# Kernel tuning notes

Measured on AMD Instinct MI355X. Metric: run time of the kernel, lower is better.

Reference implementation:

```python
import jax, jax.numpy as jnp
import numpy as np

NUM_NODES = 2048
NUM_UNITS = 64
INPUT_DIM = 2
MAX_K = 2  # max_diffusion_step


def setup_inputs() -> dict:
    key = jax.random.key(0)
    ks = jax.random.split(key, 8)
    B, N, U, D = 32, NUM_NODES, NUM_UNITS, INPUT_DIM
    C = D + U                      # input_size after concat = 66
    M = 2 * MAX_K + 1              # num_matrices = 5
    w_scale = 1.0 / np.sqrt(C * M)
    return {
        "inputs": jax.random.normal(ks[0], (B, N * D), dtype=jnp.float32),
        "hx": jax.random.normal(ks[1], (B, N * U), dtype=jnp.float32),
        # row-stochastic-ish random-walk supports (scaled so K hops stay bounded)
        "support0": jax.random.uniform(ks[2], (N, N), dtype=jnp.float32) / N,
        "support1": jax.random.uniform(ks[3], (N, N), dtype=jnp.float32) / N,
        "W_ru": jax.random.normal(ks[4], (C * M, 2 * U), dtype=jnp.float32) * w_scale,
        "b_ru": jnp.full((2 * U,), 1.0, dtype=jnp.float32),   # bias_start=1.0
        "W_c": jax.random.normal(ks[5], (C * M, U), dtype=jnp.float32) * w_scale,
        "b_c": jnp.zeros((U,), dtype=jnp.float32),            # bias_start=0.0
    }


def _gconv(inputs, state, supports, W, b, output_size):
    # inputs: [B, N*D], state: [B, N*U]
    B = inputs.shape[0]
    N = NUM_NODES
    x0 = jnp.concatenate(
        [inputs.reshape(B, N, -1), state.reshape(B, N, -1)], axis=2
    )  # [B, N, C]
    C = x0.shape[2]
    xs = [x0]
    for S in supports:  # Chebyshev-style diffusion per support
        x1 = jnp.einsum("nm,bmc->bnc", S, x0)
        xs.append(x1)
        xk1, xk2 = x1, x0
        for _ in range(2, MAX_K + 1):
            x2 = 2.0 * jnp.einsum("nm,bmc->bnc", S, xk1) - xk2
            xs.append(x2)
            xk1, xk2 = x2, xk1
    M = len(xs)  # num_matrices
    # stack on new leading axis then permute(1,2,3,0): feature-major, matrix-minor
    x = jnp.stack(xs, axis=0).transpose(1, 2, 3, 0).reshape(B * N, C * M)
    out = x @ W + b  # [B*N, output_size]
    return out.reshape(B, N * output_size)


def reference(inputs, hx, support0, support1, W_ru, b_ru, W_c, b_c):
    B = inputs.shape[0]
    N, U = NUM_NODES, NUM_UNITS
    supports = (support0, support1)
    value = jax.nn.sigmoid(_gconv(inputs, hx, supports, W_ru, b_ru, 2 * U))
    value = value.reshape(B, N, 2 * U)
    r = value[..., :U].reshape(B, N * U)
    u = value[..., U:].reshape(B, N * U)
    c = jnp.tanh(_gconv(inputs, r * hx, supports, W_c, b_c, U))
    new_state = u * hx + (1.0 - u) * c
    return new_state
```

## Files before the change

kernel.cpp:

```cpp
#include <hip/hip_runtime.h>
#include <hip/hip_bf16.h>
#include <cstdint>
#include <cstddef>

typedef unsigned short u16;
typedef unsigned char u8;
using f32x4 = __attribute__((ext_vector_type(4))) float;
using s16x8 = __attribute__((ext_vector_type(8))) short;
using s64x2 = __attribute__((ext_vector_type(2))) long;

#define NN 2048
#define BB 32
#define CC 66
#define JREAL 2112
#define JR 2176
#define KF 352
#define SROWS 65536

__device__ __forceinline__ int kperm(int k6) {
  return 16 * ((k6 >> 3) & 3) + 8 * (k6 >> 5) + (k6 & 7);
}

__device__ __forceinline__ float bf2f(u16 u) {
  union { uint32_t i; float f; } v; v.i = ((uint32_t)u) << 16; return v.f;
}
__device__ __forceinline__ u16 f2bf(float f) {
  union { float f; uint32_t i; } v; v.f = f;
  uint32_t x = v.i;
  x += 0x7fffu + ((x >> 16) & 1u);
  return (u16)(x >> 16);
}
__device__ __forceinline__ u8 f2e4m3(float x) {
  union { float f; uint32_t i; } v; v.f = x;
  uint32_t s = (v.i >> 24) & 0x80u;
  float a = fabsf(x);
  if (a >= 464.0f) return (u8)(s | 0x7Eu);
  if (a < 0.015625f) {
    int q = (int)rintf(a * 512.0f);
    return (u8)(s | (uint32_t)q);
  }
  union { float f; uint32_t i; } u; u.f = a;
  uint32_t lsb = (u.i >> 20) & 1u;
  u.i += 0x0007FFFFu + lsb;
  int e = (int)(u.i >> 23) - 127;
  uint32_t m = (u.i >> 20) & 7u;
  return (u8)(s | ((uint32_t)(e + 7) << 3) | m);
}

__device__ __forceinline__ void async_cp16(const u8* g, u8* l) {
  __builtin_amdgcn_global_load_lds(
      (const __attribute__((address_space(1))) unsigned int*)g,
      (__attribute__((address_space(3))) unsigned int*)l, 16, 0, 0);
}
__device__ __forceinline__ void async_cp16u(const u16* g, u16* l) {
  __builtin_amdgcn_global_load_lds(
      (const __attribute__((address_space(1))) unsigned int*)g,
      (__attribute__((address_space(3))) unsigned int*)l, 16, 0, 0);
}

template <int EPI>
__global__ __launch_bounds__(512, 2) void gemm_f8(
    const u8* __restrict__ A0, const u8* __restrict__ A1,
    const u8* __restrict__ A2, const u8* __restrict__ A3,
    const u8* __restrict__ B0, const u8* __restrict__ B1,
    const u8* __restrict__ B2, const u8* __restrict__ B3,
    void* __restrict__ C0, void* __restrict__ C1,
    void* __restrict__ C2, void* __restrict__ C3,
    int K, int lda, int ldb, int ldout, int mlimit)
{
  __shared__ u8 lds[3 * 25600];

  const int gx = gridDim.x, gy = gridDim.y;
  const int nwg = gx * gy * gridDim.z;
  const int orig = blockIdx.x + gx * (blockIdx.y + gy * blockIdx.z);
  const int cpx = nwg >> 3;
  const int swz = (orig & 7) * cpx + (orig >> 3);
  const int mb = swz % gx;
  const int t1 = swz / gx;
  const int nb = t1 % gy;
  const int zb = t1 / gy;

  const u8* A = (zb == 0) ? A0 : (zb == 1) ? A1 : (zb == 2) ? A2 : A3;
  const u8* B = (zb == 0) ? B0 : (zb == 1) ? B1 : (zb == 2) ? B2 : B3;
  void* Cv    = (zb == 0) ? C0 : (zb == 1) ? C1 : (zb == 2) ? C2 : C3;

  const int tid = threadIdx.x;
  const int wid = tid >> 6;
  const int lane = tid & 63;
  const int m0 = mb * 128;
  const int n0 = nb * 256;
  const int wm = (wid >> 2) * 64;
  const int wn = (wid & 3) * 64;

  const bool xtra = (EPI == 5) && (mb < 4);
  const int xrow0 = 2048 + mb * 16;
  const bool xw = xtra && (wid == 0);
  const bool xm = xtra && (wid < 4);

  const int srow = wid * 16 + (lane >> 2);
  const int sk   = ((lane & 3) ^ ((lane >> 3) & 3)) * 16;
  const u8* gA = A + (size_t)(m0 + srow) * lda + sk;
  const u8* gB = B + (size_t)(n0 + srow) * ldb + sk;
  const u8* gAx = A + (size_t)(xrow0 + (lane >> 2)) * lda + sk;
  u8* ldsA  = &lds[wid * 1024];
  u8* ldsB0 = &lds[8192 + wid * 1024];
  u8* ldsB1 = &lds[16384 + wid * 1024];
  u8* ldsAx = &lds[24576];

  const int r16 = lane & 15;
  const int hi = lane >> 4;
  const int rq = (r16 >> 1) & 3;
  const int goff = (hi ^ rq) * 16;
  const int abase = (wm + r16) * 64 + goff;
  const int bbase = 8192 + (wn + r16) * 64 + goff;
  const int xbase = 24576 + r16 * 64 + goff;

  f32x4 acc[4][4] = {};
  f32x4 accx[4] = {};
  const int nt = K >> 6;

#define STAGE_ALL(T_, SO_) { const int k0_ = (T_) * 64;                      \
    async_cp16(gA + k0_, ldsA + (SO_));                                      \
    async_cp16(gB + k0_, ldsB0 + (SO_));                                     \
    async_cp16(gB + (size_t)128 * ldb + k0_, ldsB1 + (SO_));                 \
    if (xw) async_cp16(gAx + k0_, ldsAx + (SO_)); }

  STAGE_ALL(0, 0);
  STAGE_ALL(1, 25600);
  if (xw) { asm volatile("s_waitcnt vmcnt(4)" ::: "memory"); }
  else    { asm volatile("s_waitcnt vmcnt(3)" ::: "memory"); }
  __builtin_amdgcn_s_barrier();

  int scur = 0;
  for (int t = 0; t < nt; ++t) {
    const int soff = scur * 25600;
    const bool more = (t + 2) < nt;
    int sst = scur + 2; if (sst >= 3) sst -= 3;
    const int so2 = sst * 25600;
    const int k2 = (t + 2) * 64;

    s64x2 af[4], bq, axf;

#pragma unroll
    for (int mi = 0; mi < 4; ++mi)
      af[mi] = *(const s64x2*)&lds[soff + abase + mi * 1024];
    bq = *(const s64x2*)&lds[soff + bbase];
    if (xm) axf = *(const s64x2*)&lds[soff + xbase];
    if (more) async_cp16(gA + k2, ldsA + so2);
    __builtin_amdgcn_s_barrier();
    asm volatile("s_waitcnt lgkmcnt(0)" ::: "memory");
    __builtin_amdgcn_s_setprio(1);
#pragma unroll
    for (int h = 0; h < 2; ++h) {
#pragma unroll
      for (int mi = 0; mi < 4; ++mi)
        acc[mi][0] = __builtin_amdgcn_mfma_f32_16x16x32_fp8_fp8(
            af[mi][h], bq[h], acc[mi][0], 0, 0, 0);
      if (xm) accx[0] = __builtin_amdgcn_mfma_f32_16x16x32_fp8_fp8(
            axf[h], bq[h], accx[0], 0, 0, 0);
    }
    __builtin_amdgcn_s_setprio(0);
    __builtin_amdgcn_s_barrier();

    bq = *(const s64x2*)&lds[soff + bbase + 1024];
    if (more) async_cp16(gB + k2, ldsB0 + so2);
    __builtin_amdgcn_s_barrier();
    asm volatile("s_waitcnt lgkmcnt(0)" ::: "memory");
    __builtin_amdgcn_s_setprio(1);
#pragma unroll
    for (int h = 0; h < 2; ++h) {
#pragma unroll
      for (int mi = 0; mi < 4; ++mi)
        acc[mi][1] = __builtin_amdgcn_mfma_f32_16x16x32_fp8_fp8(
            af[mi][h], bq[h], acc[mi][1], 0, 0, 0);
      if (xm) accx[1] = __builtin_amdgcn_mfma_f32_16x16x32_fp8_fp8(
            axf[h], bq[h], accx[1], 0, 0, 0);
    }
    __builtin_amdgcn_s_setprio(0);
    __builtin_amdgcn_s_barrier();

    bq = *(const s64x2*)&lds[soff + bbase + 2048];
    if (more) async_cp16(gB + (size_t)128 * ldb + k2, ldsB1 + so2);
    __builtin_amdgcn_s_barrier();
    asm volatile("s_waitcnt lgkmcnt(0)" ::: "memory");
    __builtin_amdgcn_s_setprio(1);
#pragma unroll
    for (int h = 0; h < 2; ++h) {
#pragma unroll
      for (int mi = 0; mi < 4; ++mi)
        acc[mi][2] = __builtin_amdgcn_mfma_f32_16x16x32_fp8_fp8(
            af[mi][h], bq[h], acc[mi][2], 0, 0, 0);
      if (xm) accx[2] = __builtin_amdgcn_mfma_f32_16x16x32_fp8_fp8(
            axf[h], bq[h], accx[2], 0, 0, 0);
    }
    __builtin_amdgcn_s_setprio(0);
    __builtin_amdgcn_s_barrier();

    bq = *(const s64x2*)&lds[soff + bbase + 3072];
    if (more && xw) async_cp16(gAx + k2, ldsAx + so2);
    __builtin_amdgcn_s_barrier();
    asm volatile("s_waitcnt lgkmcnt(0)" ::: "memory");
    __builtin_amdgcn_s_setprio(1);
#pragma unroll
    for (int h = 0; h < 2; ++h) {
#pragma unroll
      for (int mi = 0; mi < 4; ++mi)
        acc[mi][3] = __builtin_amdgcn_mfma_f32_16x16x32_fp8_fp8(
            af[mi][h], bq[h], acc[mi][3], 0, 0, 0);
      if (xm) accx[3] = __builtin_amdgcn_mfma_f32_16x16x32_fp8_fp8(
            axf[h], bq[h], accx[3], 0, 0, 0);
    }
    __builtin_amdgcn_s_setprio(0);
    if (more) {
      if (xw) { asm volatile("s_waitcnt vmcnt(4)" ::: "memory"); }
      else    { asm volatile("s_waitcnt vmcnt(3)" ::: "memory"); }
    } else {
      asm volatile("s_waitcnt vmcnt(0)" ::: "memory");
    }
    __builtin_amdgcn_s_barrier();
    scur = (scur + 1 == 3) ? 0 : scur + 1;
  }
#undef STAGE_ALL

  const int lr = (lane >> 4) * 4;
  const int lc = lane & 15;

  if (EPI == 5) {
    u16* tl = (u16*)lds;
    u16* xc = (u16*)Cv;
    if (xm) {
#pragma unroll
      for (int ni = 0; ni < 4; ++ni) {
        const int ng = n0 + wn + ni * 16 + lc;
#pragma unroll
        for (int r = 0; r < 4; ++r) {
          const int c = xrow0 + lr + r - 2046;
          xc[((size_t)31 * NN + ng) * KF + (size_t)(zb + 1) * CC + c] =
              f2bf(accx[ni][r] * 0.00390625f);
        }
      }
    }
#pragma unroll
    for (int half = 0; half < 2; ++half) {
      __syncthreads();
      if ((wn >> 7) == half) {
#pragma unroll
        for (int mi = 0; mi < 4; ++mi)
#pragma unroll
          for (int ni = 0; ni < 4; ++ni) {
            const int np = (wn & 127) + ni * 16 + lc;
#pragma unroll
            for (int r = 0; r < 4; ++r) {
              const int j = wm + mi * 16 + lr + r;
              tl[np * 130 + j] = f2bf(acc[mi][ni][r] * 0.00390625f);
            }
          }
      }
      __syncthreads();
      for (int p = 0; p < 32; ++p) {
        const int idx = p * 512 + tid;
        const int jj = idx & 127;
        const int np = idx >> 7;
        const int j = m0 + jj;
        if (j < JREAL) {
          const int b = j / CC;
          const int c = j - b * CC;
          const int ng = n0 + half * 128 + np;
          xc[((size_t)b * NN + ng) * KF + (size_t)(zb + 1) * CC + c] =
              tl[np * 130 + jj];
        }
      }
    }
  } else {
#pragma unroll
    for (int mi = 0; mi < 4; ++mi)
#pragma unroll
      for (int ni = 0; ni < 4; ++ni) {
        const int colg = n0 + wn + ni * 16 + lc;
#pragma unroll
        for (int r = 0; r < 4; ++r) {
          const int rowg = m0 + wm + mi * 16 + lr + r;
          if (rowg < mlimit) {
            if (EPI == 0) {
              ((u16*)Cv)[(size_t)rowg * ldout + colg] =
                  f2bf(acc[mi][ni][r] * 0.00390625f);
            } else {
              float v = acc[mi][ni][r] * 0.0078125f -
                        ((rowg == colg) ? 256.0f : 0.0f);
              const int cpk = (colg & ~63) + kperm(colg & 63);
              ((u8*)Cv)[(size_t)rowg * ldout + cpk] = f2e4m3(v);
            }
          }
        }
      }
  }
}

__global__ __launch_bounds__(512, 2) void gemm_f8T(
    const u8* __restrict__ A0, const u8* __restrict__ A1,
    const u8* __restrict__ B0, const u8* __restrict__ B1,
    u8* __restrict__ C0, u8* __restrict__ C1,
    int K, int lda, int ldb, int ldout)
{
  __shared__ u8 lds[3 * 16384];

  const int gx = gridDim.x, gy = gridDim.y;
  const int nwg = gx * gy * gridDim.z;
  const int orig = blockIdx.x + gx * (blockIdx.y + gy * blockIdx.z);
  const int cpx = nwg >> 3;
  const int swz = (orig & 7) * cpx + (orig >> 3);
  const int mb = swz % gx;
  const int t1 = swz / gx;
  const int nb = t1 % gy;
  const int zb = t1 / gy;

  const u8* A = zb ? A1 : A0;
  const u8* B = zb ? B1 : B0;
  u8* C = zb ? C1 : C0;

  const int tid = threadIdx.x;
  const int wid = tid >> 6;
  const int lane = tid & 63;
  const int m0 = mb * 128;
  const int n0 = nb * 128;
  const int wm = (wid >> 2) * 64;
  const int wn = (wid & 3) * 32;

  const int srow = wid * 16 + (lane >> 2);
  const int sk   = ((lane & 3) ^ ((lane >> 3) & 3)) * 16;
  const u8* gA = A + (size_t)(m0 + srow) * lda + sk;
  const u8* gB = B + (size_t)(n0 + srow) * ldb + sk;
  u8* ldsA = &lds[wid * 1024];
  u8* ldsB = &lds[8192 + wid * 1024];

  const int r16 = lane & 15;
  const int hi = lane >> 4;
  const int rq = (r16 >> 1) & 3;
  const int goff = (hi ^ rq) * 16;
  const int abase = (wm + r16) * 64 + goff;
  const int bbase = 8192 + (wn + r16) * 64 + goff;

  f32x4 acc[4][2] = {};
  const int nt = K >> 6;

#define STAGE(T_, SO_) { const int k0_ = (T_) * 64;                          \
    async_cp16(gA + k0_, ldsA + (SO_));                                      \
    async_cp16(gB + k0_, ldsB + (SO_)); }

  STAGE(0, 0);
  STAGE(1, 16384);
  asm volatile("s_waitcnt vmcnt(2)" ::: "memory");
  __builtin_amdgcn_s_barrier();

  int scur = 0;
  for (int t = 0; t < nt; ++t) {
    const int soff = scur * 16384;
    const bool more = (t + 2) < nt;
    if (more) {
      int sst = scur + 2; if (sst >= 3) sst -= 3;
      STAGE(t + 2, sst * 16384);
    }
    s64x2 af[4], bfr[2];
#pragma unroll
    for (int mi = 0; mi < 4; ++mi)
      af[mi] = *(const s64x2*)&lds[soff + abase + mi * 1024];
#pragma unroll
    for (int ni = 0; ni < 2; ++ni)
      bfr[ni] = *(const s64x2*)&lds[soff + bbase + ni * 1024];
    __builtin_amdgcn_s_setprio(1);
#pragma unroll
    for (int h = 0; h < 2; ++h)
#pragma unroll
      for (int mi = 0; mi < 4; ++mi)
#pragma unroll
        for (int ni = 0; ni < 2; ++ni)
          acc[mi][ni] = __builtin_amdgcn_mfma_f32_16x16x32_fp8_fp8(
              af[mi][h], bfr[ni][h], acc[mi][ni], 0, 0, 0);
    __builtin_amdgcn_s_setprio(0);
    if (more) { asm volatile("s_waitcnt vmcnt(2)" ::: "memory"); }
    else      { asm volatile("s_waitcnt vmcnt(0)" ::: "memory"); }
    __builtin_amdgcn_s_barrier();
    scur = (scur + 1 == 3) ? 0 : scur + 1;
  }
#undef STAGE

  const int lr = (lane >> 4) * 4;
  const int lc = lane & 15;
#pragma unroll
  for (int mi = 0; mi < 4; ++mi)
#pragma unroll
    for (int ni = 0; ni < 2; ++ni) {
      const int colg = n0 + wn + ni * 16 + lc;
      const int cpk = (colg & ~63) + kperm(colg & 63);
#pragma unroll
      for (int r = 0; r < 4; ++r) {
        const int rowg = m0 + wm + mi * 16 + lr + r;
        float v = acc[mi][ni][r] * 0.0078125f -
                  ((rowg == colg) ? 256.0f : 0.0f);
        C[(size_t)rowg * ldout + cpk] = f2e4m3(v);
      }
    }
}

template <int EPI>
__global__ __launch_bounds__(256) void gemm_dense(
    const u16* __restrict__ A, const u16* __restrict__ B, u16* __restrict__ C,
    const float* __restrict__ bias,
    int K, int lda, int ldb, int ldout, int nstore)
{
  __shared__ u16 At[128 * 32];
  __shared__ u16 Bt[128 * 32];
  const int nwg = gridDim.x;
  const int orig = blockIdx.x;
  const int cpx = nwg >> 3;
  const int swz = (orig & 7) * cpx + (orig >> 3);
  const int mb = swz;

  const int tid = threadIdx.x;
  const int wid = tid >> 6;
  const int lane = tid & 63;
  const int m0 = mb * 128;
  const int wm = (wid >> 1) * 64;
  const int wn = (wid & 1) * 64;
  const int rA = lane >> 2;
  const int kA = ((lane & 3) ^ ((lane >> 3) & 3)) * 8;

  f32x4 acc[4][4] = {};

  const int c0 = wid * 2, c1 = wid * 2 + 1;
  const u16* gA0 = A + (size_t)(m0 + c0 * 16 + rA) * lda + kA;
  const u16* gA1 = A + (size_t)(m0 + c1 * 16 + rA) * lda + kA;
  const u16* gB0 = B + (size_t)(c0 * 16 + rA) * ldb + kA;
  const u16* gB1 = B + (size_t)(c1 * 16 + rA) * ldb + kA;

  for (int k0 = 0; k0 < K; k0 += 32) {
    async_cp16u(gA0 + k0, &At[c0 * 512]);
    async_cp16u(gA1 + k0, &At[c1 * 512]);
    async_cp16u(gB0 + k0, &Bt[c0 * 512]);
    async_cp16u(gB1 + k0, &Bt[c1 * 512]);
    __syncthreads();
    s16x8 af[4], bfr[4];
    const int r16 = lane & 15;
    const int cswz = ((lane >> 4) ^ ((r16 >> 1) & 3)) << 3;
#pragma unroll
    for (int mi = 0; mi < 4; ++mi)
      af[mi] = *(const s16x8*)&At[(wm + mi * 16 + r16) * 32 + cswz];
#pragma unroll
    for (int ni = 0; ni < 4; ++ni)
      bfr[ni] = *(const s16x8*)&Bt[(wn + ni * 16 + r16) * 32 + cswz];
#pragma unroll
    for (int mi = 0; mi < 4; ++mi)
#pragma unroll
      for (int ni = 0; ni < 4; ++ni)
        acc[mi][ni] = __builtin_amdgcn_mfma_f32_16x16x32_bf16(af[mi], bfr[ni], acc[mi][ni], 0, 0, 0);
    __syncthreads();
  }

  const int lr = (lane >> 4) * 4;
  const int lc = lane & 15;
#pragma unroll
  for (int mi = 0; mi < 4; ++mi) {
#pragma unroll
    for (int ni = 0; ni < 4; ++ni) {
      const int colg = wn + ni * 16 + lc;
#pragma unroll
      for (int r = 0; r < 4; ++r) {
        const int rowg = m0 + wm + mi * 16 + lr + r;
        float v = acc[mi][ni][r];
        if (EPI == 2) { v += bias[colg]; v = 1.0f / (1.0f + __expf(-v)); }
        if (EPI == 3) { v += bias[colg]; v = tanhf(v); }
        if (colg < nstore)
          C[(size_t)rowg * ldout + colg] = f2bf(v);
      }
    }
  }
}

__global__ __launch_bounds__(256) void cvt_S(const float* __restrict__ Sa,
                                             const float* __restrict__ Sb,
                                             u8* __restrict__ Sha, u8* __restrict__ Shb,
                                             u8* __restrict__ Sta, u8* __restrict__ Stb) {
  __shared__ u8 tile[64 * 68];
  const float* S = blockIdx.z ? Sb : Sa;
  u8* Sh = blockIdx.z ? Shb : Sha;
  u8* St = blockIdx.z ? Stb : Sta;
  const int c0 = blockIdx.x * 64;
  const int r0 = blockIdx.y * 64;
  const int t = threadIdx.x;
#pragma unroll
  for (int p = 0; p < 4; ++p) {
    const int idx = p * 256 + t;
    const int r = idx >> 4;
    const int c4 = (idx & 15) * 4;
    float4 v = *reinterpret_cast<const float4*>(S + (size_t)(r0 + r) * NN + c0 + c4);
    union { u8 b[4]; uint32_t w; } o;
    o.b[0] = f2e4m3(v.x * 256.0f); o.b[1] = f2e4m3(v.y * 256.0f);
    o.b[2] = f2e4m3(v.z * 256.0f); o.b[3] = f2e4m3(v.w * 256.0f);
    *reinterpret_cast<uint32_t*>(Sh + (size_t)(r0 + r) * NN + c0 + kperm(c4)) = o.w;
    *reinterpret_cast<uint32_t*>(&tile[r * 68 + c4]) = o.w;
  }
  __syncthreads();
  const int cc = t >> 2;
#pragma unroll
  for (int half = 0; half < 2; ++half) {
    const int j = (t & 3) * 2 + half;
    union { u8 b[8]; uint64_t w; } buf;
#pragma unroll
    for (int i = 0; i < 8; ++i) buf.b[i] = tile[(j * 8 + i) * 68 + cc];
    const int npos = 16 * (j & 3) + 8 * (j >> 2);
    *reinterpret_cast<uint64_t*>(St + (size_t)(c0 + cc) * NN + r0 + npos) = buf.w;
  }
}

__global__ __launch_bounds__(256) void build_wt(const float* __restrict__ W,
                                                u16* __restrict__ Wt, int ocols) {
  int t = blockIdx.x * 256 + threadIdx.x;
  if (t >= 128 * KF) return;
  int o = t / KF, kf = t - o * KF;
  float v = 0.0f;
  if (kf < 330 && o < ocols) {
    int m = kf / CC, c = kf - m * CC;
    v = W[(size_t)(c * 5 + m) * ocols + o];
  }
  Wt[t] = f2bf(v);
}

__global__ __launch_bounds__(256) void pack_x0(const float* __restrict__ inputs,
                                               const float* __restrict__ hx,
                                               const u16* __restrict__ ru,
                                               u8* __restrict__ X0t,
                                               u16* __restrict__ xcat, int useR) {
  __shared__ u16 tile[128 * 76];
  const int n0 = blockIdx.x * 128;
  const int b = blockIdx.y;
  const int t = threadIdx.x;
#pragma unroll
  for (int p = 0; p < 8; ++p) {
    const int idx = p * 256 + t;
    const int n = idx >> 4;
    const int u4 = (idx & 15) * 4;
    float4 v = *reinterpret_cast<const float4*>(
        hx + (size_t)b * (NN * 64) + (size_t)(n0 + n) * 64 + u4);
    if (useR) {
      ushort4 rv = *reinterpret_cast<const ushort4*>(
          ru + ((size_t)b * NN + n0 + n) * 128 + u4);
      v.x *= bf2f(rv.x); v.y *= bf2f(rv.y); v.z *= bf2f(rv.z); v.w *= bf2f(rv.w);
    }
    ushort4 o;
    o.x = f2bf(v.x); o.y = f2bf(v.y); o.z = f2bf(v.z); o.w = f2bf(v.w);
    *reinterpret_cast<ushort4*>(&tile[n * 76 + u4]) = o;
  }
  __syncthreads();
#pragma unroll
  for (int p = 0; p < 33; ++p) {
    const int idx = p * 256 + t;
    const int c = idx >> 7;
    const int n = idx & 127;
    float val;
    if (c < 2) val = inputs[(size_t)b * (NN * 2) + (size_t)(n0 + n) * 2 + c];
    else       val = bf2f(tile[n * 76 + (c - 2)]);
    const int np = (n & ~63) + kperm(n & 63);
    X0t[(size_t)(b * CC + c) * NN + n0 + np] = f2e4m3(val);
  }
#pragma unroll
  for (int p = 0; p < 17; ++p) {
    const int idx = p * 256 + t;
    if (idx < 128 * 33) {
      const int n = idx / 33;
      const int pr = idx - n * 33;
      const int col = pr * 2;
      u16 v0, v1;
      if (col == 0) {
        v0 = f2bf(inputs[(size_t)b * (NN * 2) + (size_t)(n0 + n) * 2 + 0]);
        v1 = f2bf(inputs[(size_t)b * (NN * 2) + (size_t)(n0 + n) * 2 + 1]);
      } else {
        v0 = tile[n * 76 + (col - 2)];
        v1 = tile[n * 76 + (col - 1)];
      }
      ushort2 o2; o2.x = v0; o2.y = v1;
      *reinterpret_cast<ushort2*>(
          xcat + ((size_t)b * NN + n0 + n) * KF + col) = o2;
    }
  }
}

__global__ __launch_bounds__(256) void final_k(const float* __restrict__ hx,
                                               const u16* __restrict__ ru,
                                               const u16* __restrict__ cd,
                                               float* __restrict__ out) {
  size_t t = (size_t)blockIdx.x * 256 + threadIdx.x;
  int u = (int)(t & 63);
  size_t s = t >> 6;
  float ug = bf2f(ru[s * 128 + 64 + u]);
  float cv = bf2f(cd[s * 64 + u]);
  float h = hx[t];
  out[t] = ug * h + (1.0f - ug) * cv;
}

extern "C" void kernel_launch(void* const* d_in, const int* in_sizes, int n_in,
                              void* d_out, int out_size, void* d_ws, size_t ws_size,
                              hipStream_t stream) {
  const float* inputs = (const float*)d_in[0];
  const float* hx     = (const float*)d_in[1];
  const float* S0     = (const float*)d_in[2];
  const float* S1     = (const float*)d_in[3];
  const float* Wru    = (const float*)d_in[4];
  const float* bru    = (const float*)d_in[5];
  const float* Wc     = (const float*)d_in[6];
  const float* bc     = (const float*)d_in[7];
  float* out = (float*)d_out;

  u8* ws8 = (u8*)d_ws;
  u8* S0h = ws8;
  u8* S1h = S0h + (size_t)NN * NN;
  u8* X0t = S1h + (size_t)NN * NN;
  u16* xcat = (u16*)(X0t + (size_t)JR * NN);
  u16* Wtru = xcat + (size_t)SROWS * KF;
  u16* Wtc  = Wtru + (size_t)128 * KF;
  u16* ru   = Wtc + (size_t)128 * KF;
  u16* cd   = ru + (size_t)SROWS * 128;
  u8* S0t = (u8*)xcat;
  u8* S1t = S0t + (size_t)NN * NN;
  u8* T0 = (u8*)d_out;
  u8* T1 = T0 + (size_t)NN * NN;

  dim3 b256(256);
  dim3 b512(512);
  cvt_S<<<dim3(NN / 64, NN / 64, 2), b256, 0, stream>>>(S0, S1, S0h, S1h, S0t, S1t);
  build_wt<<<dim3((128 * KF + 255) / 256), b256, 0, stream>>>(Wru, Wtru, 128);
  build_wt<<<dim3((128 * KF + 255) / 256), b256, 0, stream>>>(Wc, Wtc, 64);

  gemm_f8T<<<dim3(NN / 128, NN / 128, 2), b512, 0, stream>>>(
      S0h, S1h, S0t, S1t, T0, T1, NN, NN, NN, NN);

  const dim3 gdiff(16, NN / 256, 4);
  const dim3 gdense(SROWS / 128);
  const dim3 gpx0(NN / 128, BB);

  pack_x0<<<gpx0, b256, 0, stream>>>(inputs, hx, (const u16*)nullptr, X0t, xcat, 0);
  gemm_f8<5><<<gdiff, b512, 0, stream>>>(
      X0t, X0t, X0t, X0t,  S0h, T0, S1h, T1,
      (void*)xcat, (void*)xcat, (void*)xcat, (void*)xcat,
      NN, NN, NN, KF, JREAL);
  gemm_dense<2><<<gdense, b256, 0, stream>>>(xcat, Wtru, ru, bru, KF, KF, KF, 128, 128);

  pack_x0<<<gpx0, b256, 0, stream>>>(inputs, hx, ru, X0t, xcat, 1);
  gemm_f8<5><<<gdiff, b512, 0, stream>>>(
      X0t, X0t, X0t, X0t,  S0h, T0, S1h, T1,
      (void*)xcat, (void*)xcat, (void*)xcat, (void*)xcat,
      NN, NN, NN, KF, JREAL);
  gemm_dense<3><<<gdense, b256, 0, stream>>>(xcat, Wtc, cd, bc, KF, KF, KF, 64, 64);

  final_k<<<dim3(SROWS * 64 / 256), b256, 0, stream>>>(hx, ru, cd, out);
}
```

Before: 237.8 us.

## Restructure fp8 GEMM phase pipelining and fuse GRU combine into dense epilogue

After: 270.8 us. +13.9%, slower.

```diff
diff --git a/kernel.cpp b/kernel.cpp
--- a/kernel.cpp
+++ b/kernel.cpp
@@ -139,76 +139,64 @@
     const int so2 = sst * 25600;
     const int k2 = (t + 2) * 64;
 
-    s64x2 af[4], bq, axf;
+    s64x2 af[4], bq0, bq1, axf;
 
 #pragma unroll
     for (int mi = 0; mi < 4; ++mi)
       af[mi] = *(const s64x2*)&lds[soff + abase + mi * 1024];
-    bq = *(const s64x2*)&lds[soff + bbase];
+    bq0 = *(const s64x2*)&lds[soff + bbase];
+    bq1 = *(const s64x2*)&lds[soff + bbase + 1024];
     if (xm) axf = *(const s64x2*)&lds[soff + xbase];
-    if (more) async_cp16(gA + k2, ldsA + so2);
+    if (more) {
+      async_cp16(gA + k2, ldsA + so2);
+      async_cp16(gB + k2, ldsB0 + so2);
+    }
     __builtin_amdgcn_s_barrier();
     asm volatile("s_waitcnt lgkmcnt(0)" ::: "memory");
     __builtin_amdgcn_s_setprio(1);
 #pragma unroll
     for (int h = 0; h < 2; ++h) {
 #pragma unroll
-      for (int mi = 0; mi < 4; ++mi)
+      for (int mi = 0; mi < 4; ++mi) {
         acc[mi][0] = __builtin_amdgcn_mfma_f32_16x16x32_fp8_fp8(
-            af[mi][h], bq[h], acc[mi][0], 0, 0, 0);
-      if (xm) accx[0] = __builtin_amdgcn_mfma_f32_16x16x32_fp8_fp8(
-            axf[h], bq[h], accx[0], 0, 0, 0);
+            af[mi][h], bq0[h], acc[mi][0], 0, 0, 0);
+        acc[mi][1] = __builtin_amdgcn_mfma_f32_16x16x32_fp8_fp8(
+            af[mi][h], bq1[h], acc[mi][1], 0, 0, 0);
+      }
+      if (xm) {
+        accx[0] = __builtin_amdgcn_mfma_f32_16x16x32_fp8_fp8(
+            axf[h], bq0[h], accx[0], 0, 0, 0);
+        accx[1] = __builtin_amdgcn_mfma_f32_16x16x32_fp8_fp8(
+            axf[h], bq1[h], accx[1], 0, 0, 0);
+      }
     }
     __builtin_amdgcn_s_setprio(0);
     __builtin_amdgcn_s_barrier();
 
-    bq = *(const s64x2*)&lds[soff + bbase + 1024];
-    if (more) async_cp16(gB + k2, ldsB0 + so2);
+    bq0 = *(const s64x2*)&lds[soff + bbase + 2048];
+    bq1 = *(const s64x2*)&lds[soff + bbase + 3072];
+    if (more) {
+      async_cp16(gB + (size_t)128 * ldb + k2, ldsB1 + so2);
+      if (xw) async_cp16(gAx + k2, ldsAx + so2);
+    }
     __builtin_amdgcn_s_barrier();
     asm volatile("s_waitcnt lgkmcnt(0)" ::: "memory");
     __builtin_amdgcn_s_setprio(1);
 #pragma unroll
     for (int h = 0; h < 2; ++h) {
 #pragma unroll
-      for (int mi = 0; mi < 4; ++mi)
-        acc[mi][1] = __builtin_amdgcn_mfma_f32_16x16x32_fp8_fp8(
-            af[mi][h], bq[h], acc[mi][1], 0, 0, 0);
-      if (xm) accx[1] = __builtin_amdgcn_mfma_f32_16x16x32_fp8_fp8(
-            axf[h], bq[h], accx[1], 0, 0, 0);
-    }
-    __builtin_amdgcn_s_setprio(0);
-    __builtin_amdgcn_s_barrier();
-
-    bq = *(const s64x2*)&lds[soff + bbase + 2048];
-    if (more) async_cp16(gB + (size_t)128 * ldb + k2, ldsB1 + so2);
-    __builtin_amdgcn_s_barrier();
-    asm volatile("s_waitcnt lgkmcnt(0)" ::: "memory");
-    __builtin_amdgcn_s_setprio(1);
-#pragma unroll
-    for (int h = 0; h < 2; ++h) {
-#pragma unroll
-      for (int mi = 0; mi < 4; ++mi)
+      for (int mi = 0; mi < 4; ++mi) {
         acc[mi][2] = __builtin_amdgcn_mfma_f32_16x16x32_fp8_fp8(
-            af[mi][h], bq[h], acc[mi][2], 0, 0, 0);
-      if (xm) accx[2] = __builtin_amdgcn_mfma_f32_16x16x32_fp8_fp8(
-            axf[h], bq[h], accx[2], 0, 0, 0);
-    }
-    __builtin_amdgcn_s_setprio(0);
-    __builtin_amdgcn_s_barrier();
-
-    bq = *(const s64x2*)&lds[soff + bbase + 3072];
-    if (more && xw) async_cp16(gAx + k2, ldsAx + so2);
-    __builtin_amdgcn_s_barrier();
-    asm volatile("s_waitcnt lgkmcnt(0)" ::: "memory");
-    __builtin_amdgcn_s_setprio(1);
-#pragma unroll
-    for (int h = 0; h < 2; ++h) {
-#pragma unroll
-      for (int mi = 0; mi < 4; ++mi)
+            af[mi][h], bq0[h], acc[mi][2], 0, 0, 0);
         acc[mi][3] = __builtin_amdgcn_mfma_f32_16x16x32_fp8_fp8(
-            af[mi][h], bq[h], acc[mi][3], 0, 0, 0);
-      if (xm) accx[3] = __builtin_amdgcn_mfma_f32_16x16x32_fp8_fp8(
-            axf[h], bq[h], accx[3], 0, 0, 0);
+            af[mi][h], bq1[h], acc[mi][3], 0, 0, 0);
+      }
+      if (xm) {
+        accx[2] = __builtin_amdgcn_mfma_f32_16x16x32_fp8_fp8(
+            axf[h], bq0[h], accx[2], 0, 0, 0);
+        accx[3] = __builtin_amdgcn_mfma_f32_16x16x32_fp8_fp8(
+            axf[h], bq1[h], accx[3], 0, 0, 0);
+      }
     }
     __builtin_amdgcn_s_setprio(0);
     if (more) {
@@ -356,26 +344,40 @@
   for (int t = 0; t < nt; ++t) {
     const int soff = scur * 16384;
     const bool more = (t + 2) < nt;
-    if (more) {
-      int sst = scur + 2; if (sst >= 3) sst -= 3;
-      STAGE(t + 2, sst * 16384);
-    }
-    s64x2 af[4], bfr[2];
+    int sst = scur + 2; if (sst >= 3) sst -= 3;
+    const int so2 = sst * 16384;
+    const int k2 = (t + 2) * 64;
+
+    s64x2 af[4], bq;
+
 #pragma unroll
     for (int mi = 0; mi < 4; ++mi)
       af[mi] = *(const s64x2*)&lds[soff + abase + mi * 1024];
-#pragma unroll
-    for (int ni = 0; ni < 2; ++ni)
-      bfr[ni] = *(const s64x2*)&lds[soff + bbase + ni * 1024];
+    bq = *(const s64x2*)&lds[soff + bbase];
+    if (more) async_cp16(gA + k2, ldsA + so2);
+    __builtin_amdgcn_s_barrier();
+    asm volatile("s_waitcnt lgkmcnt(0)" ::: "memory");
     __builtin_amdgcn_s_setprio(1);
 #pragma unroll
     for (int h = 0; h < 2; ++h)
 #pragma unroll
       for (int mi = 0; mi < 4; ++mi)
-#pragma unroll
-        for (int ni = 0; ni < 2; ++ni)
-          acc[mi][ni] = __builtin_amdgcn_mfma_f32_16x16x32_fp8_fp8(
-              af[mi][h], bfr[ni][h], acc[mi][ni], 0, 0, 0);
+        acc[mi][0] = __builtin_amdgcn_mfma_f32_16x16x32_fp8_fp8(
+            af[mi][h], bq[h], acc[mi][0], 0, 0, 0);
+    __builtin_amdgcn_s_setprio(0);
+    __builtin_amdgcn_s_barrier();
+
+    bq = *(const s64x2*)&lds[soff + bbase + 1024];
+    if (more) async_cp16(gB + k2, ldsB + so2);
+    __builtin_amdgcn_s_barrier();
+    asm volatile("s_waitcnt lgkmcnt(0)" ::: "memory");
+    __builtin_amdgcn_s_setprio(1);
+#pragma unroll
+    for (int h = 0; h < 2; ++h)
+#pragma unroll
+      for (int mi = 0; mi < 4; ++mi)
+        acc[mi][1] = __builtin_amdgcn_mfma_f32_16x16x32_fp8_fp8(
+            af[mi][h], bq[h], acc[mi][1], 0, 0, 0);
     __builtin_amdgcn_s_setprio(0);
     if (more) { asm volatile("s_waitcnt vmcnt(2)" ::: "memory"); }
     else      { asm volatile("s_waitcnt vmcnt(0)" ::: "memory"); }
@@ -406,6 +408,8 @@
 __global__ __launch_bounds__(256) void gemm_dense(
     const u16* __restrict__ A, const u16* __restrict__ B, u16* __restrict__ C,
     const float* __restrict__ bias,
+    const u16* __restrict__ rug, const float* __restrict__ hxg,
+    float* __restrict__ outg,
     int K, int lda, int ldb, int ldout, int nstore)
 {
   __shared__ u16 At[128 * 32];
@@ -467,10 +471,20 @@
       for (int r = 0; r < 4; ++r) {
         const int rowg = m0 + wm + mi * 16 + lr + r;
         float v = acc[mi][ni][r];
-        if (EPI == 2) { v += bias[colg]; v = 1.0f / (1.0f + __expf(-v)); }
-        if (EPI == 3) { v += bias[colg]; v = tanhf(v); }
-        if (colg < nstore)
-          C[(size_t)rowg * ldout + colg] = f2bf(v);
+        if (EPI == 2) {
+          v += bias[colg]; v = 1.0f / (1.0f + __expf(-v));
+          if (colg < nstore)
+            C[(size_t)rowg * ldout + colg] = f2bf(v);
+        }
+        if (EPI == 3) {
+          if (colg < nstore) {
+            v += bias[colg]; v = tanhf(v);
+            const size_t s = (size_t)rowg;
+            const float ug = bf2f(rug[s * 128 + 64 + colg]);
+            const float h  = hxg[s * 64 + colg];
+            outg[s * 64 + colg] = ug * h + (1.0f - ug) * v;
+          }
+        }
       }
     }
   }
@@ -584,19 +598,6 @@
   }
 }
 
-__global__ __launch_bounds__(256) void final_k(const float* __restrict__ hx,
-                                               const u16* __restrict__ ru,
-                                               const u16* __restrict__ cd,
-                                               float* __restrict__ out) {
-  size_t t = (size_t)blockIdx.x * 256 + threadIdx.x;
-  int u = (int)(t & 63);
-  size_t s = t >> 6;
-  float ug = bf2f(ru[s * 128 + 64 + u]);
-  float cv = bf2f(cd[s * 64 + u]);
-  float h = hx[t];
-  out[t] = ug * h + (1.0f - ug) * cv;
-}
-
 extern "C" void kernel_launch(void* const* d_in, const int* in_sizes, int n_in,
                               void* d_out, int out_size, void* d_ws, size_t ws_size,
                               hipStream_t stream) {
@@ -618,7 +619,6 @@
   u16* Wtru = xcat + (size_t)SROWS * KF;
   u16* Wtc  = Wtru + (size_t)128 * KF;
   u16* ru   = Wtc + (size_t)128 * KF;
-  u16* cd   = ru + (size_t)SROWS * 128;
   u8* S0t = (u8*)xcat;
   u8* S1t = S0t + (size_t)NN * NN;
   u8* T0 = (u8*)d_out;
@@ -642,14 +642,15 @@
       X0t, X0t, X0t, X0t,  S0h, T0, S1h, T1,
       (void*)xcat, (void*)xcat, (void*)xcat, (void*)xcat,
       NN, NN, NN, KF, JREAL);
-  gemm_dense<2><<<gdense, b256, 0, stream>>>(xcat, Wtru, ru, bru, KF, KF, KF, 128, 128);
+  gemm_dense<2><<<gdense, b256, 0, stream>>>(
+      xcat, Wtru, ru, bru, (const u16*)nullptr, (const float*)nullptr,
+      (float*)nullptr, KF, KF, KF, 128, 128);
 
   pack_x0<<<gpx0, b256, 0, stream>>>(inputs, hx, ru, X0t, xcat, 1);
   gemm_f8<5><<<gdiff, b512, 0, stream>>>(
       X0t, X0t, X0t, X0t,  S0h, T0, S1h, T1,
       (void*)xcat, (void*)xcat, (void*)xcat, (void*)xcat,
       NN, NN, NN, KF, JREAL);
-  gemm_dense<3><<<gdense, b256, 0, stream>>>(xcat, Wtc, cd, bc, KF, KF, KF, 64, 64);
-
-  final_k<<<dim3(SROWS * 64 / 256), b256, 0, stream>>>(hx, ru, cd, out);
-}
+  gemm_dense<3><<<gdense, b256, 0, stream>>>(
+      xcat, Wtc, (u16*)nullptr, bc, ru, hx, out, KF, KF, KF, 64, 64);
+}
```

## Fuse r*hx repacking and final GRU update into dense GEMM epilogues

Applied to the files above, without the earlier changes.

Result: slower. 246.5 us (+3.6%).

```diff
diff --git a/kernel.cpp b/kernel.cpp
--- a/kernel.cpp
+++ b/kernel.cpp
@@ -406,10 +406,15 @@
 __global__ __launch_bounds__(256) void gemm_dense(
     const u16* __restrict__ A, const u16* __restrict__ B, u16* __restrict__ C,
     const float* __restrict__ bias,
+    const u16* __restrict__ rug, const float* __restrict__ hxg,
+    float* __restrict__ outg,
+    const float* __restrict__ inputs_, u8* __restrict__ X0t_,
+    u16* __restrict__ xcat_,
     int K, int lda, int ldb, int ldout, int nstore)
 {
   __shared__ u16 At[128 * 32];
   __shared__ u16 Bt[128 * 32];
+  __shared__ u16 Xt[(EPI == 2) ? 128 * 68 : 1];
   const int nwg = gridDim.x;
   const int orig = blockIdx.x;
   const int cpx = nwg >> 3;
@@ -467,10 +472,70 @@
       for (int r = 0; r < 4; ++r) {
         const int rowg = m0 + wm + mi * 16 + lr + r;
         float v = acc[mi][ni][r];
-        if (EPI == 2) { v += bias[colg]; v = 1.0f / (1.0f + __expf(-v)); }
-        if (EPI == 3) { v += bias[colg]; v = tanhf(v); }
-        if (colg < nstore)
-          C[(size_t)rowg * ldout + colg] = f2bf(v);
+        if (EPI == 2) {
+          v += bias[colg]; v = 1.0f / (1.0f + __expf(-v));
+          const size_t s = (size_t)rowg;
+          if (colg >= 64) {
+            C[s * 64 + (colg - 64)] = f2bf(v);
+          } else {
+            const float rq = bf2f(f2bf(v));
+            const float h  = hxg[s * 64 + colg];
+            const int nl = wm + mi * 16 + lr + r;
+            Xt[nl * 68 + colg] = f2bf(rq * h);
+          }
+        }
+        if (EPI == 3) {
+          if (colg < nstore) {
+            v += bias[colg]; v = tanhf(v);
+            const size_t s = (size_t)rowg;
+            const float ug = bf2f(rug[s * 64 + colg]);
+            const float h  = hxg[s * 64 + colg];
+            outg[s * 64 + colg] = ug * h + (1.0f - ug) * v;
+          }
+        }
+      }
+    }
+  }
+
+  if (EPI == 2) {
+    __syncthreads();
+    const int b = m0 >> 11;
+    const int np0 = m0 & 2047;
+    const int t = tid;
+    {
+      const int c = t >> 7;
+      const int n = t & 127;
+      const int np = (n & ~63) + kperm(n & 63);
+      const float val = inputs_[(size_t)b * (NN * 2) + (size_t)(np0 + n) * 2 + c];
+      X0t_[(size_t)(b * CC + c) * NN + np0 + np] = f2e4m3(val);
+    }
+#pragma unroll
+    for (int p = 0; p < 32; ++p) {
+      const int idx = p * 256 + t;
+      const int c2 = idx >> 7;
+      const int n = idx & 127;
+      const int np = (n & ~63) + kperm(n & 63);
+      X0t_[(size_t)(b * CC + 2 + c2) * NN + np0 + np] =
+          f2e4m3(bf2f(Xt[n * 68 + c2]));
+    }
+#pragma unroll
+    for (int p = 0; p < 17; ++p) {
+      const int idx = p * 256 + t;
+      if (idx < 128 * 33) {
+        const int n = idx / 33;
+        const int pr = idx - n * 33;
+        const int col = pr * 2;
+        u16 v0, v1;
+        if (col == 0) {
+          v0 = f2bf(inputs_[(size_t)b * (NN * 2) + (size_t)(np0 + n) * 2 + 0]);
+          v1 = f2bf(inputs_[(size_t)b * (NN * 2) + (size_t)(np0 + n) * 2 + 1]);
+        } else {
+          v0 = Xt[n * 68 + (col - 2)];
+          v1 = Xt[n * 68 + (col - 1)];
+        }
+        ushort2 o2; o2.x = v0; o2.y = v1;
+        *reinterpret_cast<ushort2*>(
+            xcat_ + ((size_t)b * NN + np0 + n) * KF + col) = o2;
       }
     }
   }
@@ -527,9 +592,8 @@
 
 __global__ __launch_bounds__(256) void pack_x0(const float* __restrict__ inputs,
                                                const float* __restrict__ hx,
-                                               const u16* __restrict__ ru,
                                                u8* __restrict__ X0t,
-                                               u16* __restrict__ xcat, int useR) {
+                                               u16* __restrict__ xcat) {
   __shared__ u16 tile[128 * 76];
   const int n0 = blockIdx.x * 128;
   const int b = blockIdx.y;
@@ -541,11 +605,6 @@
     const int u4 = (idx & 15) * 4;
     float4 v = *reinterpret_cast<const float4*>(
         hx + (size_t)b * (NN * 64) + (size_t)(n0 + n) * 64 + u4);
-    if (useR) {
-      ushort4 rv = *reinterpret_cast<const ushort4*>(
-          ru + ((size_t)b * NN + n0 + n) * 128 + u4);
-      v.x *= bf2f(rv.x); v.y *= bf2f(rv.y); v.z *= bf2f(rv.z); v.w *= bf2f(rv.w);
-    }
     ushort4 o;
     o.x = f2bf(v.x); o.y = f2bf(v.y); o.z = f2bf(v.z); o.w = f2bf(v.w);
     *reinterpret_cast<ushort4*>(&tile[n * 76 + u4]) = o;
@@ -584,19 +643,6 @@
   }
 }
 
-__global__ __launch_bounds__(256) void final_k(const float* __restrict__ hx,
-                                               const u16* __restrict__ ru,
-                                               const u16* __restrict__ cd,
-                                               float* __restrict__ out) {
-  size_t t = (size_t)blockIdx.x * 256 + threadIdx.x;
-  int u = (int)(t & 63);
-  size_t s = t >> 6;
-  float ug = bf2f(ru[s * 128 + 64 + u]);
-  float cv = bf2f(cd[s * 64 + u]);
-  float h = hx[t];
-  out[t] = ug * h + (1.0f - ug) * cv;
-}
-
 extern "C" void kernel_launch(void* const* d_in, const int* in_sizes, int n_in,
                               void* d_out, int out_size, void* d_ws, size_t ws_size,
                               hipStream_t stream) {
@@ -618,7 +664,6 @@
   u16* Wtru = xcat + (size_t)SROWS * KF;
   u16* Wtc  = Wtru + (size_t)128 * KF;
   u16* ru   = Wtc + (size_t)128 * KF;
-  u16* cd   = ru + (size_t)SROWS * 128;
   u8* S0t = (u8*)xcat;
   u8* S1t = S0t + (size_t)NN * NN;
   u8* T0 = (u8*)d_out;
@@ -637,19 +682,20 @@
   const dim3 gdense(SROWS / 128);
   const dim3 gpx0(NN / 128, BB);
 
-  pack_x0<<<gpx0, b256, 0, stream>>>(inputs, hx, (const u16*)nullptr, X0t, xcat, 0);
+  pack_x0<<<gpx0, b256, 0, stream>>>(inputs, hx, X0t, xcat);
   gemm_f8<5><<<gdiff, b512, 0, stream>>>(
       X0t, X0t, X0t, X0t,  S0h, T0, S1h, T1,
       (void*)xcat, (void*)xcat, (void*)xcat, (void*)xcat,
       NN, NN, NN, KF, JREAL);
-  gemm_dense<2><<<gdense, b256, 0, stream>>>(xcat, Wtru, ru, bru, KF, KF, KF, 128, 128);
-
-  pack_x0<<<gpx0, b256, 0, stream>>>(inputs, hx, ru, X0t, xcat, 1);
+  gemm_dense<2><<<gdense, b256, 0, stream>>>(
+      xcat, Wtru, ru, bru, (const u16*)nullptr, hx, (float*)nullptr,
+      inputs, X0t, xcat, KF, KF, KF, 64, 128);
+
   gemm_f8<5><<<gdiff, b512, 0, stream>>>(
       X0t, X0t, X0t, X0t,  S0h, T0, S1h, T1,
       (void*)xcat, (void*)xcat, (void*)xcat, (void*)xcat,
       NN, NN, NN, KF, JREAL);
-  gemm_dense<3><<<gdense, b256, 0, stream>>>(xcat, Wtc, cd, bc, KF, KF, KF, 64, 64);
-
-  final_k<<<dim3(SROWS * 64 / 256), b256, 0, stream>>>(hx, ru, cd, out);
-}
+  gemm_dense<3><<<gdense, b256, 0, stream>>>(
+      xcat, Wtc, (u16*)nullptr, bc, ru, hx, out,
+      (const float*)nullptr, (u8*)nullptr, (u16*)nullptr, KF, KF, KF, 64, 64);
+}
```
